# Performance work log

Measured on AMD Instinct MI355X. Metric: run time of the kernel, lower is better.

The kernel has to match this reference:

```python
import jax, jax.numpy as jnp
import numpy as np

ALPHA = 0.8  # LeakyReLU negative slope
OUT_DIM = 128
EDGE_DIM = 64


def setup_inputs() -> dict:
    key = jax.random.key(0)
    ks = jax.random.split(key, 6)
    N, NS, IN, OUT, ED = 25000, 32, 128, OUT_DIM, EDGE_DIM
    return {
        "input": jax.random.normal(ks[0], (N, IN), jnp.float32),
        "neigh_feat": jax.random.normal(ks[1], (N * NS, IN), jnp.float32),
        "edge_emb": jax.random.normal(ks[2], (N * NS, ED), jnp.float32),
        "mask": jnp.zeros((N,), jnp.int32),  # unused by forward, kept for signature fidelity
        "W": jax.random.normal(ks[3], (IN, OUT), jnp.float32) * 0.1,
        "W2": jax.random.normal(ks[4], (IN, OUT), jnp.float32) * 0.1,
        "a": jax.random.normal(ks[5], (2 * OUT + ED, 1), jnp.float32) * 0.1,
    }


def reference(input, neigh_feat, edge_emb, mask, W, W2, a):
    N = input.shape[0]
    ns = neigh_feat.shape[0] // N
    out_dim = W.shape[1]
    ed = edge_emb.shape[1]

    x = input @ W                                   # [N, out]
    neighs = (neigh_feat @ W2).reshape(N, ns, out_dim)  # [N, ns, out]
    edge = edge_emb.reshape(N, ns, ed)              # [N, ns, ed]

    # a_input @ a decomposed: avoid materializing the repeated/concatenated tensor.
    a_x = a[:out_dim, 0]
    a_n = a[out_dim:2 * out_dim, 0]
    a_e = a[2 * out_dim:, 0]
    scores = (x @ a_x)[:, None] + neighs @ a_n + edge @ a_e  # [N, ns]
    e = jnp.where(scores > 0, scores, ALPHA * scores)        # LeakyReLU(alpha)

    attention = jax.nn.softmax(e, axis=1)           # softmax over neighbors
    # dropout p=0.0 (eval) -> identity

    h_prime = jnp.einsum("ns,nsd->nd", attention, neighs)  # [N, out]
    output = jnp.concatenate([x, h_prime], axis=1)          # concat_node
    e_agg = jnp.einsum("ns,nse->ne", attention, edge)       # concat_edge
    output = jnp.concatenate([output, e_agg], axis=1)       # [N, 2*out+ed]
    return jax.nn.elu(output)
```

## Files before the change

### kernel.cpp

```cpp
#include <hip/hip_runtime.h>
#include <hip/hip_bf16.h>
#include <math.h>

typedef __bf16 bf16_t;
typedef __attribute__((ext_vector_type(8))) __bf16 bf16x8;
typedef __attribute__((ext_vector_type(4))) __bf16 bf16x4;
typedef __attribute__((ext_vector_type(4))) float f32x4;

#define NB 8

__global__ __launch_bounds__(256) void pack_weights_kernel(
    const float* __restrict__ W, const float* __restrict__ W2,
    const float* __restrict__ a,
    bf16_t* __restrict__ Wp, bf16_t* __restrict__ W2p,
    float* __restrict__ w2an, float* __restrict__ wax) {
  int idx = blockIdx.x * 256 + threadIdx.x;
  int j  = idx & 7;
  int l  = (idx >> 3) & 63;
  int nt = (idx >> 9) & 7;
  int kt = idx >> 12;
  int k   = kt * 32 + (l >> 4) * 8 + j;
  int col = nt * 16 + (l & 15);
  Wp[idx]  = (bf16_t)W[k * 128 + col];
  W2p[idx] = (bf16_t)W2[k * 128 + col];
  if (blockIdx.x == 0 && threadIdx.x < 128) {
    const float* r = W2 + threadIdx.x * 128;
    float s = 0.f;
    for (int c = 0; c < 128; ++c) s += r[c] * a[128 + c];
    w2an[threadIdx.x] = s;
  }
  if (blockIdx.x == 1 && threadIdx.x < 128) {
    const float* r = W + threadIdx.x * 128;
    float s = 0.f;
    for (int c = 0; c < 128; ++c) s += r[c] * a[c];
    wax[threadIdx.x] = s;
  }
}

__global__ __launch_bounds__(256) void node_kernel(
    const float* __restrict__ input,
    const float* __restrict__ neigh_feat, const float* __restrict__ edge_emb,
    const float* __restrict__ a, const float* __restrict__ w2an,
    const float* __restrict__ wax,
    const bf16_t* __restrict__ Wp, const bf16_t* __restrict__ W2p,
    float* __restrict__ out) {
  const int t = threadIdx.x;
  const int w = t >> 6, l = t & 63;
  const int n0 = blockIdx.x * NB;

  __shared__ __align__(16) bf16_t Ax[16 * 128];
  __shared__ __align__(16) bf16_t Ah[16 * 128];
  __shared__ float Agg[8][128];
  __shared__ float srow[32], se[32];
  __shared__ __align__(16) f32x4 nag[4][32];
  __shared__ __align__(16) f32x4 eag[4][16];
  __shared__ float sxs[8];

  const int q = l & 31;
  const int h = l >> 5;
  const int p = l & 15;
  const int g = l >> 4;

  const f32x4 wn = *(const f32x4*)(w2an + 4 * q);
  const f32x4 ae = *(const f32x4*)(a + 256 + 4 * p);

  f32x4 nA[4], eA[2], nB[4], eB[2];

#define ISSUE(P, node_) do {                                              \
    const float* nf_ = neigh_feat + (size_t)(node_) * 4096 + 4 * t;       \
    n##P[0] = *(const f32x4*)(nf_);                                       \
    n##P[1] = *(const f32x4*)(nf_ + 1024);                                \
    n##P[2] = *(const f32x4*)(nf_ + 2048);                                \
    n##P[3] = *(const f32x4*)(nf_ + 3072);                                \
    const float* ee_ = edge_emb + (size_t)(node_) * 2048 + 4 * t;         \
    e##P[0] = *(const f32x4*)(ee_);                                       \
    e##P[1] = *(const f32x4*)(ee_ + 1024);                                \
  } while (0)

  ISSUE(A, n0);
  ISSUE(B, n0 + 1);

  {
    const int r2 = t >> 5;
    const int c0 = 4 * (t & 31);
    f32x4 iv = *(const f32x4*)(input + (size_t)(n0 + r2) * 128 + c0);
    f32x4 wv = *(const f32x4*)(wax + c0);
    float s = iv[0]*wv[0] + iv[1]*wv[1] + iv[2]*wv[2] + iv[3]*wv[3];
    s += __shfl_xor(s, 1);  s += __shfl_xor(s, 2);  s += __shfl_xor(s, 4);
    s += __shfl_xor(s, 8);  s += __shfl_xor(s, 16);
    if ((l & 31) == 0) sxs[r2] = s;
    bf16x4 b;
#pragma unroll
    for (int j = 0; j < 4; ++j) b[j] = (bf16_t)iv[j];
    const int gg = (t & 31) >> 1;
    *(bf16x4*)(&Ax[r2 * 128 + ((gg ^ r2) << 3) + 4 * (t & 1)]) = b;
    bf16x4 z = {(bf16_t)0.f, (bf16_t)0.f, (bf16_t)0.f, (bf16_t)0.f};
    *(bf16x4*)(&Ax[1024 + 4 * t]) = z;
    *(bf16x4*)(&Ah[1024 + 4 * t]) = z;
  }
  __syncthreads();

  {
    const int arow = l & 15;
    f32x4 acc0 = {}, acc1 = {};
#pragma unroll
    for (int kt = 0; kt < 4; ++kt) {
      bf16x8 af = *(const bf16x8*)(&Ax[arow * 128 + ((kt * 32 + (l >> 4) * 8) ^ ((arow & 7) << 3))]);
      bf16x8 b0 = *(const bf16x8*)(&Wp[((kt * 8 + 2 * w) * 64 + l) * 8]);
      bf16x8 b1 = *(const bf16x8*)(&Wp[((kt * 8 + 2 * w + 1) * 64 + l) * 8]);
      acc0 = __builtin_amdgcn_mfma_f32_16x16x32_bf16(af, b0, acc0, 0, 0, 0);
      acc1 = __builtin_amdgcn_mfma_f32_16x16x32_bf16(af, b1, acc1, 0, 0, 0);
    }
    if ((l >> 4) < 2) {
#pragma unroll
      for (int j = 0; j < 4; ++j) {
        int row = (l >> 4) * 4 + j;
        float v0 = acc0[j];
        v0 = v0 > 0.f ? v0 : __expf(v0) - 1.f;
        __builtin_nontemporal_store(v0, out + (size_t)(n0 + row) * 320 + 2 * w * 16 + (l & 15));
        float v1 = acc1[j];
        v1 = v1 > 0.f ? v1 : __expf(v1) - 1.f;
        __builtin_nontemporal_store(v1, out + (size_t)(n0 + row) * 320 + (2 * w + 1) * 16 + (l & 15));
      }
    }
  }

#define BODY(P, kk) do {                                                  \
    const int node = n0 + (kk);                                           \
    _Pragma("unroll")                                                     \
    for (int j = 0; j < 4; ++j) {                                         \
      float s = n##P[j][0]*wn[0] + n##P[j][1]*wn[1]                       \
              + n##P[j][2]*wn[2] + n##P[j][3]*wn[3];                      \
      s += __shfl_xor(s, 1);  s += __shfl_xor(s, 2);                      \
      s += __shfl_xor(s, 4);  s += __shfl_xor(s, 8);                      \
      s += __shfl_xor(s, 16);                                             \
      if (q == 0) srow[8*j + 2*w + h] = s;                                \
    }                                                                     \
    _Pragma("unroll")                                                     \
    for (int j = 0; j < 2; ++j) {                                         \
      float s = e##P[j][0]*ae[0] + e##P[j][1]*ae[1]                       \
              + e##P[j][2]*ae[2] + e##P[j][3]*ae[3];                      \
      s += __shfl_xor(s, 1);  s += __shfl_xor(s, 2);                      \
      s += __shfl_xor(s, 4);  s += __shfl_xor(s, 8);                      \
      if (p == 0) se[16*j + 4*w + g] = s;                                 \
    }                                                                     \
    __syncthreads();                                                      \
    float av;                                                             \
    {                                                                     \
      float e0 = srow[q] + se[q] + sxs[kk];                               \
      e0 = e0 > 0.f ? e0 : 0.8f * e0;                                     \
      float m = e0;                                                       \
      m = fmaxf(m, __shfl_xor(m, 1));                                     \
      m = fmaxf(m, __shfl_xor(m, 2));                                     \
      m = fmaxf(m, __shfl_xor(m, 4));                                     \
      m = fmaxf(m, __shfl_xor(m, 8));                                     \
      m = fmaxf(m, __shfl_xor(m, 16));                                    \
      float pe = __expf(e0 - m);                                          \
      float s2 = pe;                                                      \
      s2 += __shfl_xor(s2, 1);                                            \
      s2 += __shfl_xor(s2, 2);                                            \
      s2 += __shfl_xor(s2, 4);                                            \
      s2 += __shfl_xor(s2, 8);                                            \
      s2 += __shfl_xor(s2, 16);                                           \
      av = pe / s2;                                                       \
    }                                                                     \
    {                                                                     \
      f32x4 pn = {0.f, 0.f, 0.f, 0.f};                                    \
      _Pragma("unroll")                                                   \
      for (int j = 0; j < 4; ++j) {                                       \
        float as = __shfl(av, 8*j + 2*w + h);                             \
        pn += as * n##P[j];                                               \
      }                                                                   \
      pn[0] += __shfl_xor(pn[0], 32);                                     \
      pn[1] += __shfl_xor(pn[1], 32);                                     \
      pn[2] += __shfl_xor(pn[2], 32);                                     \
      pn[3] += __shfl_xor(pn[3], 32);                                     \
      if (h == 0) nag[w][q] = pn;                                         \
      f32x4 pv = {0.f, 0.f, 0.f, 0.f};                                    \
      _Pragma("unroll")                                                   \
      for (int j = 0; j < 2; ++j) {                                       \
        float as = __shfl(av, 16*j + 4*w + g);                            \
        pv += as * e##P[j];                                               \
      }                                                                   \
      pv[0] += __shfl_xor(pv[0], 16);                                     \
      pv[1] += __shfl_xor(pv[1], 16);                                     \
      pv[2] += __shfl_xor(pv[2], 16);                                     \
      pv[3] += __shfl_xor(pv[3], 16);                                     \
      pv[0] += __shfl_xor(pv[0], 32);                                     \
      pv[1] += __shfl_xor(pv[1], 32);                                     \
      pv[2] += __shfl_xor(pv[2], 32);                                     \
      pv[3] += __shfl_xor(pv[3], 32);                                     \
      if (l < 16) eag[w][p] = pv;                                         \
    }                                                                     \
    if ((kk) + 2 < NB) ISSUE(P, node + 2);                                \
    __syncthreads();                                                      \
    if (t < 128) {                                                        \
      const float* f = (const float*)nag;                                 \
      Agg[kk][t] = f[t] + f[128 + t] + f[256 + t] + f[384 + t];           \
    } else if (t < 192) {                                                 \
      int c = t - 128;                                                    \
      const float* f = (const float*)eag;                                 \
      float v = f[c] + f[64 + c] + f[128 + c] + f[192 + c];               \
      v = v > 0.f ? v : __expf(v) - 1.f;                                  \
      __builtin_nontemporal_store(v, out + (size_t)node * 320 + 256 + c); \
    }                                                                     \
  } while (0)

#pragma unroll 1
  for (int k = 0; k < NB; k += 2) {
    BODY(A, k);
    BODY(B, k + 1);
  }
#undef BODY
#undef ISSUE

  __syncthreads();

  {
    const int r2 = t >> 5;
    const int c0 = 4 * (t & 31);
    f32x4 v = *(const f32x4*)(&Agg[r2][c0]);
    bf16x4 b;
#pragma unroll
    for (int j = 0; j < 4; ++j) b[j] = (bf16_t)v[j];
    const int gg = (t & 31) >> 1;
    *(bf16x4*)(&Ah[r2 * 128 + ((gg ^ r2) << 3) + 4 * (t & 1)]) = b;
  }
  __syncthreads();
  {
    const int arow = l & 15;
    f32x4 acc0 = {}, acc1 = {};
#pragma unroll
    for (int kt = 0; kt < 4; ++kt) {
      bf16x8 af = *(const bf16x8*)(&Ah[arow * 128 + ((kt * 32 + (l >> 4) * 8) ^ ((arow & 7) << 3))]);
      bf16x8 b0 = *(const bf16x8*)(&W2p[((kt * 8 + 2 * w) * 64 + l) * 8]);
      bf16x8 b1 = *(const bf16x8*)(&W2p[((kt * 8 + 2 * w + 1) * 64 + l) * 8]);
      acc0 = __builtin_amdgcn_mfma_f32_16x16x32_bf16(af, b0, acc0, 0, 0, 0);
      acc1 = __builtin_amdgcn_mfma_f32_16x16x32_bf16(af, b1, acc1, 0, 0, 0);
    }
    if ((l >> 4) < 2) {
#pragma unroll
      for (int j = 0; j < 4; ++j) {
        int row = (l >> 4) * 4 + j;
        float v0 = acc0[j];
        v0 = v0 > 0.f ? v0 : __expf(v0) - 1.f;
        __builtin_nontemporal_store(v0, out + (size_t)(n0 + row) * 320 + 128 + 2 * w * 16 + (l & 15));
        float v1 = acc1[j];
        v1 = v1 > 0.f ? v1 : __expf(v1) - 1.f;
        __builtin_nontemporal_store(v1, out + (size_t)(n0 + row) * 320 + 128 + (2 * w + 1) * 16 + (l & 15));
      }
    }
  }
}

extern "C" void kernel_launch(void* const* d_in, const int* in_sizes, int n_in,
                              void* d_out, int out_size, void* d_ws, size_t ws_size,
                              hipStream_t stream) {
  const float* input = (const float*)d_in[0];
  const float* neigh = (const float*)d_in[1];
  const float* edge  = (const float*)d_in[2];
  const float* W     = (const float*)d_in[4];
  const float* W2    = (const float*)d_in[5];
  const float* a     = (const float*)d_in[6];
  float* out = (float*)d_out;

  const int N = in_sizes[0] / 128;

  bf16_t* W2p  = (bf16_t*)d_ws;
  bf16_t* Wp   = W2p + 16384;
  float*  w2an = (float*)((char*)d_ws + 65536);
  float*  wax  = (float*)((char*)d_ws + 66048);

  pack_weights_kernel<<<64, 256, 0, stream>>>(W, W2, a, Wp, W2p, w2an, wax);
  node_kernel<<<N / NB, 256, 0, stream>>>(input, neigh, edge, a, w2an, wax,
                                          Wp, W2p, out);
}
```

Before: 149.7 us.

## Single-buffer neighbor prefetch, merge LDS tiles, raise occupancy hint

Replaces the two-deep register prefetch (A/B buffers, two nodes in flight) with a single buffer that prefetches the next node after the current node's reductions. The Ax and Ah shared-memory tiles are merged into one reused buffer, and launch_bounds asks for 5 blocks per CU. Together these cut register and LDS use to fit more resident waves, which should hide memory latency through occupancy. In exchange each wave has less memory-level parallelism, since only one node's loads are in flight at a time.

Result: no change. 147.5 us (-1.5%).

```diff
diff --git a/kernel.cpp b/kernel.cpp
--- a/kernel.cpp
+++ b/kernel.cpp
@@ -37,7 +37,7 @@
   }
 }
 
-__global__ __launch_bounds__(256) void node_kernel(
+__global__ __launch_bounds__(256, 5) void node_kernel(
     const float* __restrict__ input,
     const float* __restrict__ neigh_feat, const float* __restrict__ edge_emb,
     const float* __restrict__ a, const float* __restrict__ w2an,
@@ -48,8 +48,7 @@
   const int w = t >> 6, l = t & 63;
   const int n0 = blockIdx.x * NB;
 
-  __shared__ __align__(16) bf16_t Ax[16 * 128];
-  __shared__ __align__(16) bf16_t Ah[16 * 128];
+  __shared__ __align__(16) bf16_t AxAh[16 * 128];
   __shared__ float Agg[8][128];
   __shared__ float srow[32], se[32];
   __shared__ __align__(16) f32x4 nag[4][32];
@@ -64,21 +63,20 @@
   const f32x4 wn = *(const f32x4*)(w2an + 4 * q);
   const f32x4 ae = *(const f32x4*)(a + 256 + 4 * p);
 
-  f32x4 nA[4], eA[2], nB[4], eB[2];
-
-#define ISSUE(P, node_) do {                                              \
+  f32x4 nA[4], eA[2];
+
+#define ISSUE(node_) do {                                                 \
     const float* nf_ = neigh_feat + (size_t)(node_) * 4096 + 4 * t;       \
-    n##P[0] = *(const f32x4*)(nf_);                                       \
-    n##P[1] = *(const f32x4*)(nf_ + 1024);                                \
-    n##P[2] = *(const f32x4*)(nf_ + 2048);                                \
-    n##P[3] = *(const f32x4*)(nf_ + 3072);                                \
+    nA[0] = *(const f32x4*)(nf_);                                         \
+    nA[1] = *(const f32x4*)(nf_ + 1024);                                  \
+    nA[2] = *(const f32x4*)(nf_ + 2048);                                  \
+    nA[3] = *(const f32x4*)(nf_ + 3072);                                  \
     const float* ee_ = edge_emb + (size_t)(node_) * 2048 + 4 * t;         \
-    e##P[0] = *(const f32x4*)(ee_);                                       \
-    e##P[1] = *(const f32x4*)(ee_ + 1024);                                \
+    eA[0] = *(const f32x4*)(ee_);                                         \
+    eA[1] = *(const f32x4*)(ee_ + 1024);                                  \
   } while (0)
 
-  ISSUE(A, n0);
-  ISSUE(B, n0 + 1);
+  ISSUE(n0);
 
   {
     const int r2 = t >> 5;
@@ -93,10 +91,9 @@
 #pragma unroll
     for (int j = 0; j < 4; ++j) b[j] = (bf16_t)iv[j];
     const int gg = (t & 31) >> 1;
-    *(bf16x4*)(&Ax[r2 * 128 + ((gg ^ r2) << 3) + 4 * (t & 1)]) = b;
+    *(bf16x4*)(&AxAh[r2 * 128 + ((gg ^ r2) << 3) + 4 * (t & 1)]) = b;
     bf16x4 z = {(bf16_t)0.f, (bf16_t)0.f, (bf16_t)0.f, (bf16_t)0.f};
-    *(bf16x4*)(&Ax[1024 + 4 * t]) = z;
-    *(bf16x4*)(&Ah[1024 + 4 * t]) = z;
+    *(bf16x4*)(&AxAh[1024 + 4 * t]) = z;
   }
   __syncthreads();
 
@@ -105,7 +102,7 @@
     f32x4 acc0 = {}, acc1 = {};
 #pragma unroll
     for (int kt = 0; kt < 4; ++kt) {
-      bf16x8 af = *(const bf16x8*)(&Ax[arow * 128 + ((kt * 32 + (l >> 4) * 8) ^ ((arow & 7) << 3))]);
+      bf16x8 af = *(const bf16x8*)(&AxAh[arow * 128 + ((kt * 32 + (l >> 4) * 8) ^ ((arow & 7) << 3))]);
       bf16x8 b0 = *(const bf16x8*)(&Wp[((kt * 8 + 2 * w) * 64 + l) * 8]);
       bf16x8 b1 = *(const bf16x8*)(&Wp[((kt * 8 + 2 * w + 1) * 64 + l) * 8]);
       acc0 = __builtin_amdgcn_mfma_f32_16x16x32_bf16(af, b0, acc0, 0, 0, 0);
@@ -125,93 +122,90 @@
     }
   }
 
-#define BODY(P, kk) do {                                                  \
-    const int node = n0 + (kk);                                           \
-    _Pragma("unroll")                                                     \
-    for (int j = 0; j < 4; ++j) {                                         \
-      float s = n##P[j][0]*wn[0] + n##P[j][1]*wn[1]                       \
-              + n##P[j][2]*wn[2] + n##P[j][3]*wn[3];                      \
-      s += __shfl_xor(s, 1);  s += __shfl_xor(s, 2);                      \
-      s += __shfl_xor(s, 4);  s += __shfl_xor(s, 8);                      \
-      s += __shfl_xor(s, 16);                                             \
-      if (q == 0) srow[8*j + 2*w + h] = s;                                \
-    }                                                                     \
-    _Pragma("unroll")                                                     \
-    for (int j = 0; j < 2; ++j) {                                         \
-      float s = e##P[j][0]*ae[0] + e##P[j][1]*ae[1]                       \
-              + e##P[j][2]*ae[2] + e##P[j][3]*ae[3];                      \
-      s += __shfl_xor(s, 1);  s += __shfl_xor(s, 2);                      \
-      s += __shfl_xor(s, 4);  s += __shfl_xor(s, 8);                      \
-      if (p == 0) se[16*j + 4*w + g] = s;                                 \
-    }                                                                     \
-    __syncthreads();                                                      \
-    float av;                                                             \
-    {                                                                     \
-      float e0 = srow[q] + se[q] + sxs[kk];                               \
-      e0 = e0 > 0.f ? e0 : 0.8f * e0;                                     \
-      float m = e0;                                                       \
-      m = fmaxf(m, __shfl_xor(m, 1));                                     \
-      m = fmaxf(m, __shfl_xor(m, 2));                                     \
-      m = fmaxf(m, __shfl_xor(m, 4));                                     \
-      m = fmaxf(m, __shfl_xor(m, 8));                                     \
-      m = fmaxf(m, __shfl_xor(m, 16));                                    \
-      float pe = __expf(e0 - m);                                          \
-      float s2 = pe;                                                      \
-      s2 += __shfl_xor(s2, 1);                                            \
-      s2 += __shfl_xor(s2, 2);                                            \
-      s2 += __shfl_xor(s2, 4);                                            \
-      s2 += __shfl_xor(s2, 8);                                            \
-      s2 += __shfl_xor(s2, 16);                                           \
-      av = pe / s2;                                                       \
-    }                                                                     \
-    {                                                                     \
-      f32x4 pn = {0.f, 0.f, 0.f, 0.f};                                    \
-      _Pragma("unroll")                                                   \
-      for (int j = 0; j < 4; ++j) {                                       \
-        float as = __shfl(av, 8*j + 2*w + h);                             \
-        pn += as * n##P[j];                                               \
-      }                                                                   \
-      pn[0] += __shfl_xor(pn[0], 32);                                     \
-      pn[1] += __shfl_xor(pn[1], 32);                                     \
-      pn[2] += __shfl_xor(pn[2], 32);                                     \
-      pn[3] += __shfl_xor(pn[3], 32);                                     \
-      if (h == 0) nag[w][q] = pn;                                         \
-      f32x4 pv = {0.f, 0.f, 0.f, 0.f};                                    \
-      _Pragma("unroll")                                                   \
-      for (int j = 0; j < 2; ++j) {                                       \
-        float as = __shfl(av, 16*j + 4*w + g);                            \
-        pv += as * e##P[j];                                               \
-      }                                                                   \
-      pv[0] += __shfl_xor(pv[0], 16);                                     \
-      pv[1] += __shfl_xor(pv[1], 16);                                     \
-      pv[2] += __shfl_xor(pv[2], 16);                                     \
-      pv[3] += __shfl_xor(pv[3], 16);                                     \
-      pv[0] += __shfl_xor(pv[0], 32);                                     \
-      pv[1] += __shfl_xor(pv[1], 32);                                     \
-      pv[2] += __shfl_xor(pv[2], 32);                                     \
-      pv[3] += __shfl_xor(pv[3], 32);                                     \
-      if (l < 16) eag[w][p] = pv;                                         \
-    }                                                                     \
-    if ((kk) + 2 < NB) ISSUE(P, node + 2);                                \
-    __syncthreads();                                                      \
-    if (t < 128) {                                                        \
-      const float* f = (const float*)nag;                                 \
-      Agg[kk][t] = f[t] + f[128 + t] + f[256 + t] + f[384 + t];           \
-    } else if (t < 192) {                                                 \
-      int c = t - 128;                                                    \
-      const float* f = (const float*)eag;                                 \
-      float v = f[c] + f[64 + c] + f[128 + c] + f[192 + c];               \
-      v = v > 0.f ? v : __expf(v) - 1.f;                                  \
-      __builtin_nontemporal_store(v, out + (size_t)node * 320 + 256 + c); \
-    }                                                                     \
-  } while (0)
-
 #pragma unroll 1
-  for (int k = 0; k < NB; k += 2) {
-    BODY(A, k);
-    BODY(B, k + 1);
-  }
-#undef BODY
+  for (int k = 0; k < NB; ++k) {
+    const int node = n0 + k;
+
+#pragma unroll
+    for (int j = 0; j < 4; ++j) {
+      float s = nA[j][0]*wn[0] + nA[j][1]*wn[1] + nA[j][2]*wn[2] + nA[j][3]*wn[3];
+      s += __shfl_xor(s, 1);  s += __shfl_xor(s, 2);
+      s += __shfl_xor(s, 4);  s += __shfl_xor(s, 8);
+      s += __shfl_xor(s, 16);
+      if (q == 0) srow[8*j + 2*w + h] = s;
+    }
+#pragma unroll
+    for (int j = 0; j < 2; ++j) {
+      float s = eA[j][0]*ae[0] + eA[j][1]*ae[1] + eA[j][2]*ae[2] + eA[j][3]*ae[3];
+      s += __shfl_xor(s, 1);  s += __shfl_xor(s, 2);
+      s += __shfl_xor(s, 4);  s += __shfl_xor(s, 8);
+      if (p == 0) se[16*j + 4*w + g] = s;
+    }
+    __syncthreads();
+
+    float av;
+    {
+      float e0 = srow[q] + se[q] + sxs[k];
+      e0 = e0 > 0.f ? e0 : 0.8f * e0;
+      float m = e0;
+      m = fmaxf(m, __shfl_xor(m, 1));
+      m = fmaxf(m, __shfl_xor(m, 2));
+      m = fmaxf(m, __shfl_xor(m, 4));
+      m = fmaxf(m, __shfl_xor(m, 8));
+      m = fmaxf(m, __shfl_xor(m, 16));
+      float pe = __expf(e0 - m);
+      float s2 = pe;
+      s2 += __shfl_xor(s2, 1);
+      s2 += __shfl_xor(s2, 2);
+      s2 += __shfl_xor(s2, 4);
+      s2 += __shfl_xor(s2, 8);
+      s2 += __shfl_xor(s2, 16);
+      av = pe / s2;
+    }
+
+    {
+      f32x4 pn = {0.f, 0.f, 0.f, 0.f};
+#pragma unroll
+      for (int j = 0; j < 4; ++j) {
+        float as = __shfl(av, 8*j + 2*w + h);
+        pn += as * nA[j];
+      }
+      pn[0] += __shfl_xor(pn[0], 32);
+      pn[1] += __shfl_xor(pn[1], 32);
+      pn[2] += __shfl_xor(pn[2], 32);
+      pn[3] += __shfl_xor(pn[3], 32);
+      if (h == 0) nag[w][q] = pn;
+      f32x4 pv = {0.f, 0.f, 0.f, 0.f};
+#pragma unroll
+      for (int j = 0; j < 2; ++j) {
+        float as = __shfl(av, 16*j + 4*w + g);
+        pv += as * eA[j];
+      }
+      pv[0] += __shfl_xor(pv[0], 16);
+      pv[1] += __shfl_xor(pv[1], 16);
+      pv[2] += __shfl_xor(pv[2], 16);
+      pv[3] += __shfl_xor(pv[3], 16);
+      pv[0] += __shfl_xor(pv[0], 32);
+      pv[1] += __shfl_xor(pv[1], 32);
+      pv[2] += __shfl_xor(pv[2], 32);
+      pv[3] += __shfl_xor(pv[3], 32);
+      if (l < 16) eag[w][p] = pv;
+    }
+
+    if (k + 1 < NB) ISSUE(node + 1);
+    __syncthreads();
+
+    if (t < 128) {
+      const float* f = (const float*)nag;
+      Agg[k][t] = f[t] + f[128 + t] + f[256 + t] + f[384 + t];
+    } else if (t < 192) {
+      int c = t - 128;
+      const float* f = (const float*)eag;
+      float v = f[c] + f[64 + c] + f[128 + c] + f[192 + c];
+      v = v > 0.f ? v : __expf(v) - 1.f;
+      __builtin_nontemporal_store(v, out + (size_t)node * 320 + 256 + c);
+    }
+  }
 #undef ISSUE
 
   __syncthreads();
@@ -224,7 +218,7 @@
 #pragma unroll
     for (int j = 0; j < 4; ++j) b[j] = (bf16_t)v[j];
     const int gg = (t & 31) >> 1;
-    *(bf16x4*)(&Ah[r2 * 128 + ((gg ^ r2) << 3) + 4 * (t & 1)]) = b;
+    *(bf16x4*)(&AxAh[r2 * 128 + ((gg ^ r2) << 3) + 4 * (t & 1)]) = b;
   }
   __syncthreads();
   {
@@ -232,7 +226,7 @@
     f32x4 acc0 = {}, acc1 = {};
 #pragma unroll
     for (int kt = 0; kt < 4; ++kt) {
-      bf16x8 af = *(const bf16x8*)(&Ah[arow * 128 + ((kt * 32 + (l >> 4) * 8) ^ ((arow & 7) << 3))]);
+      bf16x8 af = *(const bf16x8*)(&AxAh[arow * 128 + ((kt * 32 + (l >> 4) * 8) ^ ((arow & 7) << 3))]);
       bf16x8 b0 = *(const bf16x8*)(&W2p[((kt * 8 + 2 * w) * 64 + l) * 8]);
       bf16x8 b1 = *(const bf16x8*)(&W2p[((kt * 8 + 2 * w + 1) * 64 + l) * 8]);
       acc0 = __builtin_amdgcn_mfma_f32_16x16x32_bf16(af, b0, acc0, 0, 0, 0);
```
